# Kernel tuning notes

Hardware: AMD Instinct MI355X
Metric: run time of the kernel (lower is better)

The kernel has to match this reference:

```python
import jax, jax.numpy as jnp
import numpy as np

B, S, D, H, DF = 8, 1024, 1024, 16, 4096
DK = D // H
EPS = 1e-5


def setup_inputs() -> dict:
    key = jax.random.key(0)
    ks = jax.random.split(key, 16)
    w = lambda k, shape: (jax.random.normal(k, shape, jnp.float32) * 0.02)
    inp = {
        "x": jax.random.normal(ks[0], (B, S, D), jnp.float32),
        "mask": jnp.ones((B, 1, 1, S), jnp.int32),
        # attention projections (torch Linear: y = x @ W.T + b)
        "Wq": w(ks[1], (D, D)), "bq": jnp.zeros((D,), jnp.float32),
        "Wk": w(ks[2], (D, D)), "bk": jnp.zeros((D,), jnp.float32),
        "Wv": w(ks[3], (D, D)), "bv": jnp.zeros((D,), jnp.float32),
        "Wo": w(ks[4], (D, D)), "bo": jnp.zeros((D,), jnp.float32),
        "ln_attn_g": jnp.ones((D,), jnp.float32), "ln_attn_b": jnp.zeros((D,), jnp.float32),
        # feed-forward
        "W1": w(ks[5], (DF, D)), "b1": jnp.zeros((DF,), jnp.float32),
        "W2": w(ks[6], (D, DF)), "b2": jnp.zeros((D,), jnp.float32),
        "ln_ff_g": jnp.ones((D,), jnp.float32), "ln_ff_b": jnp.zeros((D,), jnp.float32),
        # BatchNorm1d(d_ff) inside FFN (eval mode: running stats)
        "bnff_g": jnp.ones((DF,), jnp.float32), "bnff_b": jnp.zeros((DF,), jnp.float32),
        "bnff_m": jnp.zeros((DF,), jnp.float32), "bnff_v": jnp.ones((DF,), jnp.float32),
        # BatchNorm1d(d_model) after each sublayer (eval mode)
        "bn1_g": jnp.ones((D,), jnp.float32), "bn1_b": jnp.zeros((D,), jnp.float32),
        "bn1_m": jnp.zeros((D,), jnp.float32), "bn1_v": jnp.ones((D,), jnp.float32),
        "bn2_g": jnp.ones((D,), jnp.float32), "bn2_b": jnp.zeros((D,), jnp.float32),
        "bn2_m": jnp.zeros((D,), jnp.float32), "bn2_v": jnp.ones((D,), jnp.float32),
    }
    return inp


def _layernorm(x, g, b):
    mu = jnp.mean(x, axis=-1, keepdims=True)
    var = jnp.mean(jnp.square(x - mu), axis=-1, keepdims=True)
    return (x - mu) * jax.lax.rsqrt(var + EPS) * g + b


def _batchnorm_eval(x, g, b, m, v):
    # x: [B,S,C]; BatchNorm1d over channel C (the transpose->bn->transpose in torch
    # is equivalent to per-channel affine normalization on the last dim in eval mode)
    return (x - m) * jax.lax.rsqrt(v + EPS) * g + b


def reference(x, mask, Wq, bq, Wk, bk, Wv, bv, Wo, bo, ln_attn_g, ln_attn_b,
              W1, b1, W2, b2, ln_ff_g, ln_ff_b,
              bnff_g, bnff_b, bnff_m, bnff_v,
              bn1_g, bn1_b, bn1_m, bn1_v,
              bn2_g, bn2_b, bn2_m, bn2_v):
    # ---- Multi-head self-attention (pre-LN on query/key/value input) ----
    xq = _layernorm(x, ln_attn_g, ln_attn_b)
    q = (xq @ Wq.T + bq).reshape(B, S, H, DK)
    k = (x @ Wk.T + bk).reshape(B, S, H, DK)   # note: original applies LN only to `query`;
    v = (x @ Wv.T + bv).reshape(B, S, H, DK)   # key/value are passed raw (same x here)
    scores = jnp.einsum("bqhd,bkhd->bhqk", q, k) / np.sqrt(DK).astype(np.float32)
    scores = jnp.where(mask == 0, jnp.float32(-1e9), scores)
    attn = jax.nn.softmax(scores, axis=-1)                      # [B,H,S,S]
    context = jnp.einsum("bhqk,bkhd->bqhd", attn, v).reshape(B, S, D)
    attn_out = context @ Wo.T + bo
    x = x + attn_out                                            # residual (eval: no dropout)
    x = _batchnorm_eval(x, bn1_g, bn1_b, bn1_m, bn1_v)
    # ---- Position-wise FFN ----
    xn = _layernorm(x, ln_ff_g, ln_ff_b)
    h = jax.nn.gelu(xn @ W1.T + b1, approximate=False)          # [B,S,DF]
    h = _batchnorm_eval(h, bnff_g, bnff_b, bnff_m, bnff_v)
    ff = h @ W2.T + b2
    x = x + ff
    x = _batchnorm_eval(x, bn2_g, bn2_b, bn2_m, bn2_v)
    return x, attn
```

## Files before the change

### kernel.cpp

```cpp
#include <hip/hip_runtime.h>
#include <hip/hip_bf16.h>
#include <math.h>

typedef __hip_bfloat16 bf16;
typedef __attribute__((ext_vector_type(8))) short short8;
typedef __attribute__((ext_vector_type(4))) short short4v;
typedef __attribute__((ext_vector_type(4))) float f32x4;

#define DEV static __device__ __forceinline__

DEV short f2bf(float f) {
    bf16 h = __float2bfloat16(f);
    return __builtin_bit_cast(short, h);
}

DEV void glds16(const void* g, void* l) {
    __builtin_amdgcn_global_load_lds((const __attribute__((address_space(1))) void*)g,
                                     (__attribute__((address_space(3))) void*)l, 16, 0, 0);
}

__global__ __launch_bounds__(256) void cast_all(const float* __restrict__ Wq,
                                                const float* __restrict__ Wk,
                                                const float* __restrict__ Wv,
                                                const float* __restrict__ Wo,
                                                const float* __restrict__ W1,
                                                const float* __restrict__ W2,
                                                bf16* __restrict__ wqkv, bf16* __restrict__ wo,
                                                bf16* __restrict__ w1, bf16* __restrict__ w2) {
    int i = blockIdx.x * 256 + threadIdx.x;
    const float* src;
    bf16* dst;
    int si, di;
    if (i < 786432) {
        src = (i < 262144) ? Wq : (i < 524288) ? Wk : Wv;
        si = (i < 262144) ? i : (i < 524288) ? i - 262144 : i - 524288;
        dst = wqkv; di = i;
    } else if (i < 1048576) {
        src = Wo; si = i - 786432; dst = wo; di = si;
    } else if (i < 2097152) {
        src = W1; si = i - 1048576; dst = w1; di = si;
    } else {
        src = W2; si = i - 2097152; dst = w2; di = si;
    }
    f32x4 v = ((const f32x4*)src)[si];
    short4v o;
    #pragma unroll
    for (int j = 0; j < 4; j++) o[j] = f2bf(v[j]);
    ((short4v*)dst)[di] = o;
}

__global__ __launch_bounds__(256) void affine_all(
    const float* __restrict__ g1, const float* __restrict__ bb1, const float* __restrict__ m1, const float* __restrict__ v1,
    const float* __restrict__ g2, const float* __restrict__ bb2, const float* __restrict__ m2, const float* __restrict__ v2,
    const float* __restrict__ gf, const float* __restrict__ bbf, const float* __restrict__ mf, const float* __restrict__ vf,
    float* __restrict__ s1, float* __restrict__ t1, float* __restrict__ s2, float* __restrict__ t2,
    float* __restrict__ sf, float* __restrict__ tf) {
    int i = blockIdx.x * 256 + threadIdx.x;
    const float *g, *b, *m, *v; float *s, *t; int j;
    if (i < 1024)      { g = g1; b = bb1; m = m1; v = v1; s = s1; t = t1; j = i; }
    else if (i < 2048) { g = g2; b = bb2; m = m2; v = v2; s = s2; t = t2; j = i - 1024; }
    else               { g = gf; b = bbf; m = mf; v = vf; s = sf; t = tf; j = i - 2048; }
    float sc = g[j] * rsqrtf(v[j] + 1e-5f);
    s[j] = sc;
    t[j] = b[j] - m[j] * sc;
}

__global__ __launch_bounds__(256) void ln_kernel(const float* __restrict__ x,
                                                 const float* __restrict__ g,
                                                 const float* __restrict__ b,
                                                 bf16* __restrict__ lnout,
                                                 bf16* __restrict__ rawout) {
    const int row = blockIdx.x, t = threadIdx.x;
    const float* xr = x + (size_t)row * 1024;
    f32x4 v = ((const f32x4*)xr)[t];
    float s = v[0] + v[1] + v[2] + v[3];
    float sq = v[0]*v[0] + v[1]*v[1] + v[2]*v[2] + v[3]*v[3];
    #pragma unroll
    for (int off = 1; off < 64; off <<= 1) {
        s  += __shfl_xor(s, off);
        sq += __shfl_xor(sq, off);
    }
    __shared__ float ls[4], lq[4];
    if ((t & 63) == 0) { ls[t >> 6] = s; lq[t >> 6] = sq; }
    __syncthreads();
    s = ls[0] + ls[1] + ls[2] + ls[3];
    sq = lq[0] + lq[1] + lq[2] + lq[3];
    float mu = s * (1.0f / 1024.0f);
    float rs = rsqrtf(sq * (1.0f / 1024.0f) - mu * mu + 1e-5f);
    f32x4 gg = ((const f32x4*)g)[t];
    f32x4 bb = ((const f32x4*)b)[t];
    short4v o;
    #pragma unroll
    for (int j = 0; j < 4; j++) o[j] = f2bf((v[j] - mu) * rs * gg[j] + bb[j]);
    ((short4v*)(lnout + (size_t)row * 1024))[t] = o;
    if (rawout) {
        short4v r;
        #pragma unroll
        for (int j = 0; j < 4; j++) r[j] = f2bf(v[j]);
        ((short4v*)(rawout + (size_t)row * 1024))[t] = r;
    }
}

enum { M_RESBN = 0, M_GELU = 1, M_QKV = 2 };

template <int BN, int MODE>
__global__ __launch_bounds__(512, 2) void gemm8(
    const bf16* __restrict__ A0, const bf16* __restrict__ A1, const bf16* __restrict__ Bw,
    const float* __restrict__ b0, const float* __restrict__ b1, const float* __restrict__ b2,
    void* __restrict__ o0, void* __restrict__ o1, void* __restrict__ o2,
    const float* __restrict__ res, const float* __restrict__ sa, const float* __restrict__ ta,
    int N, int K) {
    constexpr int NB = BN / 64;
    constexpr int SB = BN * 128;
    constexpr int CW = BN / 4;
    constexpr int NF = CW / 16;
    __shared__ char smem[65536 + 2 * SB];

    const int tid = threadIdx.x, lane = tid & 63, wid = tid >> 6;
    const int gx = gridDim.x;
    const int n_wg = gx * gridDim.y;
    int lin = blockIdx.y * gx + blockIdx.x;
    lin = (lin & 7) * (n_wg >> 3) + (lin >> 3);
    const int bn = (lin % gx) * BN, bm = (lin / gx) << 8;

    const int wr = wid >> 2, wc = wid & 3;
    const int arow = lane & 15, hi = lane >> 4;
    const int xr = arow & 7;
    const int ck0 = (hi ^ xr) << 3;
    const int ck1 = ((4 + hi) ^ xr) << 3;
    const int rowA = wr * 128 + arow;
    const int rowB = wc * CW + arow;

    const bf16* Asel;
    if constexpr (MODE == M_QKV) Asel = (bn < 1024) ? A0 : A1;
    else                         Asel = A0;

    const int rS = tid >> 3;
    const int cXor = ((tid & 7) ^ (rS & 7)) << 3;
    const bf16* gA = Asel + (size_t)(bm + rS) * K + cXor;
    const bf16* gB = Bw   + (size_t)(bn + rS) * K + cXor;

    f32x4 acc[8][NF] = {};

    auto stA = [&](int t, int i) {
        glds16(gA + (size_t)i * 64 * K + t * 64,
               smem + ((t & 1) << 15) + i * 8192 + (wid << 10));
    };
    auto stB = [&](int t, int i) {
        glds16(gB + (size_t)i * 64 * K + t * 64,
               smem + 65536 + (t & 1) * SB + i * 8192 + (wid << 10));
    };

    const int NT = K >> 6;
    #pragma unroll
    for (int i = 0; i < NB; i++) stB(0, i);
    stA(0, 0); stA(0, 2); stA(0, 1); stA(0, 3);

#define PHASE(Q)                                                                              \
    do {                                                                                      \
        const short8 a00 = *(const short8*)(Ap + (rowA + (2*(Q)) * 16) * 64 + ck0);           \
        const short8 a01 = *(const short8*)(Ap + (rowA + (2*(Q)) * 16) * 64 + ck1);           \
        const short8 a10 = *(const short8*)(Ap + (rowA + (2*(Q)+1) * 16) * 64 + ck0);         \
        const short8 a11 = *(const short8*)(Ap + (rowA + (2*(Q)+1) * 16) * 64 + ck1);         \
        __builtin_amdgcn_s_setprio(1);                                                        \
        _Pragma("unroll")                                                                     \
        for (int n = 0; n < NF; n++) {                                                        \
            acc[2*(Q)][n]   = __builtin_amdgcn_mfma_f32_16x16x32_bf16(a00, bva[n], acc[2*(Q)][n], 0, 0, 0);   \
            acc[2*(Q)][n]   = __builtin_amdgcn_mfma_f32_16x16x32_bf16(a01, bvb[n], acc[2*(Q)][n], 0, 0, 0);   \
            acc[2*(Q)+1][n] = __builtin_amdgcn_mfma_f32_16x16x32_bf16(a10, bva[n], acc[2*(Q)+1][n], 0, 0, 0); \
            acc[2*(Q)+1][n] = __builtin_amdgcn_mfma_f32_16x16x32_bf16(a11, bvb[n], acc[2*(Q)+1][n], 0, 0, 0); \
        }                                                                                     \
        __builtin_amdgcn_s_setprio(0);                                                        \
    } while (0)

    for (int t = 0; t < NT; ++t) {
        const int p = t & 1;
        const bf16* Ap = (const bf16*)(smem + (p << 15));
        const bf16* Bp = (const bf16*)(smem + 65536 + p * SB);
        asm volatile("s_waitcnt vmcnt(2)" ::: "memory");
        __builtin_amdgcn_s_barrier();
        if (t + 1 < NT) {
            stB(t + 1, 0);
            if constexpr (NB == 4) stB(t + 1, 1);
        }
        short8 bva[NF], bvb[NF];
        #pragma unroll
        for (int n = 0; n < NF; n++) {
            bva[n] = *(const short8*)(Bp + (rowB + n * 16) * 64 + ck0);
            bvb[n] = *(const short8*)(Bp + (rowB + n * 16) * 64 + ck1);
        }
        PHASE(0);
        __builtin_amdgcn_s_barrier();
        if (t + 1 < NT) {
            if constexpr (NB == 4) { stB(t + 1, 2); stB(t + 1, 3); }
            else                   { stB(t + 1, 1); }
        }
        PHASE(1);
        if (t == NT - 1) asm volatile("s_waitcnt vmcnt(0)" ::: "memory");
        else if constexpr (NB == 4) asm volatile("s_waitcnt vmcnt(4)" ::: "memory");
        else                        asm volatile("s_waitcnt vmcnt(2)" ::: "memory");
        __builtin_amdgcn_s_barrier();
        if (t + 1 < NT) { stA(t + 1, 0); stA(t + 1, 2); }
        PHASE(2);
        __builtin_amdgcn_s_barrier();
        if (t + 1 < NT) { stA(t + 1, 1); stA(t + 1, 3); }
        PHASE(3);
    }
#undef PHASE

    #pragma unroll
    for (int mf = 0; mf < 8; mf++) {
        #pragma unroll
        for (int nf = 0; nf < NF; nf++) {
            const int col = bn + wc * CW + nf * 16 + arow;
            #pragma unroll
            for (int j = 0; j < 4; j++) {
                const int row = bm + wr * 128 + mf * 16 + hi * 4 + j;
                if constexpr (MODE == M_RESBN) {
                    float v = acc[mf][nf][j] + b0[col];
                    size_t idx = (size_t)row * N + col;
                    ((float*)o0)[idx] = (res[idx] + v) * sa[col] + ta[col];
                } else if constexpr (MODE == M_GELU) {
                    float v = acc[mf][nf][j] + b0[col];
                    float ge = 0.5f * v * (1.0f + erff(v * 0.70710678118f));
                    ((bf16*)o0)[(size_t)row * N + col] = __float2bfloat16(ge * sa[col] + ta[col]);
                } else {
                    const int reg = col >> 10, c = col & 1023;
                    const float bb = (reg == 0) ? b0[c] : (reg == 1) ? b1[c] : b2[c];
                    float v = acc[mf][nf][j] + bb;
                    if (reg == 0)
                        ((bf16*)o0)[(size_t)row * 1024 + c] = __float2bfloat16(v * 0.125f);
                    else if (reg == 1)
                        ((bf16*)o1)[(size_t)row * 1024 + c] = __float2bfloat16(v);
                    else
                        ((bf16*)o2)[((size_t)(row >> 10) << 20) + ((size_t)c << 10) + (row & 1023)] =
                            __float2bfloat16(v);
                }
            }
        }
    }
}

__global__ __launch_bounds__(512, 4) void fattn_kernel(const bf16* __restrict__ q,
                                                       const bf16* __restrict__ k,
                                                       const bf16* __restrict__ vT,
                                                       const int* __restrict__ mask,
                                                       float* __restrict__ attn,
                                                       bf16* __restrict__ ctx) {
    const int bh = blockIdx.y, b = bh >> 4, h = bh & 15;
    const int q0 = blockIdx.x << 5;
    const int tid = threadIdx.x, lane = tid & 63, wid = tid >> 6;
    const int kb = wid << 7;
    const int arow = lane & 15, hi = lane >> 4, koff = hi << 3;
    const int rbase = hi << 2;

    __shared__ char smem[67584];
    bf16* Plds = (bf16*)smem;
    float* redm = (float*)(smem + 65536);
    float* reds = (float*)(smem + 66560);

    const size_t obase = (((size_t)bh << 10) + q0) << 10;

    for (int m = 0; m < 2; m++) {
        const bf16* qp = q + ((size_t)((b << 10) + q0 + (m << 4) + arow) << 10) + (h << 6);
        const short8 qf  = *(const short8*)(qp + koff);
        const short8 qf2 = *(const short8*)(qp + 32 + koff);

        f32x4 acc[8];
        #pragma unroll
        for (int n = 0; n < 8; n++) acc[n] = (f32x4){0.f, 0.f, 0.f, 0.f};

        #pragma unroll
        for (int n = 0; n < 8; n++) {
            const bf16* kp = k + ((size_t)((b << 10) + kb + (n << 4) + arow) << 10) + (h << 6);
            short8 kf  = *(const short8*)(kp + koff);
            short8 kf2 = *(const short8*)(kp + 32 + koff);
            acc[n] = __builtin_amdgcn_mfma_f32_16x16x32_bf16(qf,  kf,  acc[n], 0, 0, 0);
            acc[n] = __builtin_amdgcn_mfma_f32_16x16x32_bf16(qf2, kf2, acc[n], 0, 0, 0);
        }

        float rmax[4];
        #pragma unroll
        for (int j = 0; j < 4; j++) rmax[j] = -3.0e38f;
        #pragma unroll
        for (int n = 0; n < 8; n++) {
            const float madd = mask[(b << 10) + kb + (n << 4) + arow] ? 0.0f : -1e9f;
            #pragma unroll
            for (int j = 0; j < 4; j++) {
                acc[n][j] += madd;
                rmax[j] = fmaxf(rmax[j], acc[n][j]);
            }
        }
        #pragma unroll
        for (int off = 1; off < 16; off <<= 1)
            #pragma unroll
            for (int j = 0; j < 4; j++) rmax[j] = fmaxf(rmax[j], __shfl_xor(rmax[j], off));

        if (arow == 0) {
            #pragma unroll
            for (int j = 0; j < 4; j++) redm[(((m << 4) + rbase + j) << 3) + wid] = rmax[j];
        }
        __syncthreads();
        #pragma unroll
        for (int j = 0; j < 4; j++) {
            const float* rr = redm + (((m << 4) + rbase + j) << 3);
            f32x4 r0 = *(const f32x4*)rr, r1 = *(const f32x4*)(rr + 4);
            rmax[j] = fmaxf(fmaxf(fmaxf(r0[0], r0[1]), fmaxf(r0[2], r0[3])),
                            fmaxf(fmaxf(r1[0], r1[1]), fmaxf(r1[2], r1[3])));
        }

        float rsum[4] = {0.f, 0.f, 0.f, 0.f};
        #pragma unroll
        for (int n = 0; n < 8; n++)
            #pragma unroll
            for (int j = 0; j < 4; j++) {
                float p = __expf(acc[n][j] - rmax[j]);
                acc[n][j] = p;
                rsum[j] += p;
            }
        #pragma unroll
        for (int off = 1; off < 16; off <<= 1)
            #pragma unroll
            for (int j = 0; j < 4; j++) rsum[j] += __shfl_xor(rsum[j], off);

        if (arow == 0) {
            #pragma unroll
            for (int j = 0; j < 4; j++) reds[(((m << 4) + rbase + j) << 3) + wid] = rsum[j];
        }
        __syncthreads();
        float inv[4];
        #pragma unroll
        for (int j = 0; j < 4; j++) {
            const float* rr = reds + (((m << 4) + rbase + j) << 3);
            f32x4 r0 = *(const f32x4*)rr, r1 = *(const f32x4*)(rr + 4);
            inv[j] = 1.0f / (r0[0] + r0[1] + r0[2] + r0[3] + r1[0] + r1[1] + r1[2] + r1[3]);
        }

        #pragma unroll
        for (int j = 0; j < 4; j++) {
            const int qr = (m << 4) + rbase + j;
            float* orow = attn + obase + ((size_t)qr << 10) + kb;
            char* prow = (char*)Plds + (qr << 11);
            const int rx = (qr & 7) << 4;
            const float iv = inv[j];
            #pragma unroll
            for (int n = 0; n < 8; n++) {
                float p = acc[n][j] * iv;
                orow[(n << 4) + arow] = p;
                *(bf16*)(prow + ((((kb + (n << 4) + arow)) << 1) ^ rx)) = __float2bfloat16(p);
            }
        }
    }

    asm volatile("s_waitcnt lgkmcnt(0)" ::: "memory");
    __builtin_amdgcn_s_barrier();
    __builtin_amdgcn_sched_barrier(0);

    const int qh = wid >> 2, dh = wid & 3;
    const char* pbase = (char*)Plds + (((qh << 4) + arow) << 11);
    const int prx = (arow & 7) << 4;
    const bf16* vrow = vT + ((size_t)((b << 10) + (h << 6) + (dh << 4) + arow) << 10);
    f32x4 acc2 = (f32x4){0.f, 0.f, 0.f, 0.f};
    #pragma unroll 8
    for (int kt = 0; kt < 32; kt++) {
        short8 af  = *(const short8*)(pbase + (((kt << 6) + (hi << 4)) ^ prx));
        short8 bf2 = *(const short8*)(vrow + (kt << 5) + koff);
        acc2 = __builtin_amdgcn_mfma_f32_16x16x32_bf16(af, bf2, acc2, 0, 0, 0);
    }

    #pragma unroll
    for (int j = 0; j < 4; j++) {
        const int row = q0 + (qh << 4) + rbase + j;
        ctx[((size_t)((b << 10) + row) << 10) + (h << 6) + (dh << 4) + arow] =
            __float2bfloat16(acc2[j]);
    }
}

extern "C" void kernel_launch(void* const* d_in, const int* in_sizes, int n_in,
                              void* d_out, int out_size, void* d_ws, size_t ws_size,
                              hipStream_t stream) {
    (void)in_sizes; (void)n_in; (void)out_size; (void)ws_size;
    const float* x   = (const float*)d_in[0];
    const int*   mask= (const int*)d_in[1];
    const float* Wq  = (const float*)d_in[2];  const float* bq  = (const float*)d_in[3];
    const float* Wk  = (const float*)d_in[4];  const float* bk  = (const float*)d_in[5];
    const float* Wv  = (const float*)d_in[6];  const float* bv  = (const float*)d_in[7];
    const float* Wo  = (const float*)d_in[8];  const float* bo  = (const float*)d_in[9];
    const float* lag = (const float*)d_in[10]; const float* lab = (const float*)d_in[11];
    const float* W1  = (const float*)d_in[12]; const float* b1  = (const float*)d_in[13];
    const float* W2  = (const float*)d_in[14]; const float* b2  = (const float*)d_in[15];
    const float* lfg = (const float*)d_in[16]; const float* lfb = (const float*)d_in[17];
    const float* bffg= (const float*)d_in[18]; const float* bffb= (const float*)d_in[19];
    const float* bffm= (const float*)d_in[20]; const float* bffv= (const float*)d_in[21];
    const float* b1g = (const float*)d_in[22]; const float* b1b = (const float*)d_in[23];
    const float* b1m = (const float*)d_in[24]; const float* b1v = (const float*)d_in[25];
    const float* b2g = (const float*)d_in[26]; const float* b2b = (const float*)d_in[27];
    const float* b2m = (const float*)d_in[28]; const float* b2v = (const float*)d_in[29];

    char* ws = (char*)d_ws;
    const size_t MB = 1024 * 1024;
    bf16* wqkv_bf = (bf16*)(ws);
    bf16* wo_bf   = (bf16*)(ws + 6 * MB);
    bf16* w1_bf   = (bf16*)(ws + 8 * MB);
    bf16* w2_bf   = (bf16*)(ws + 16 * MB);
    float* s1  = (float*)(ws + 24 * MB); float* t1  = s1 + 1024;
    float* s2  = t1 + 1024;              float* t2  = s2 + 1024;
    float* sff = t2 + 1024;              float* tff = sff + 4096;
    bf16* x_bf   = (bf16*)(ws + 25 * MB);
    bf16* xq_bf  = (bf16*)(ws + 41 * MB);
    bf16* q_bf   = (bf16*)(ws + 57 * MB);
    bf16* k_bf   = (bf16*)(ws + 73 * MB);
    bf16* vT_bf  = (bf16*)(ws + 89 * MB);
    bf16* ctx_bf = (bf16*)(ws + 105 * MB);
    float* x1    = (float*)(ws + 121 * MB);
    bf16* xn_bf  = (bf16*)(ws + 153 * MB);
    bf16* h_bf   = (bf16*)(ws + 169 * MB);

    float* out_x    = (float*)d_out;
    float* out_attn = out_x + (size_t)8 * 1024 * 1024;

    cast_all<<<12288, 256, 0, stream>>>(Wq, Wk, Wv, Wo, W1, W2, wqkv_bf, wo_bf, w1_bf, w2_bf);
    affine_all<<<24, 256, 0, stream>>>(b1g, b1b, b1m, b1v, b2g, b2b, b2m, b2v,
                                       bffg, bffb, bffm, bffv, s1, t1, s2, t2, sff, tff);

    ln_kernel<<<8192, 256, 0, stream>>>(x, lag, lab, xq_bf, x_bf);

    gemm8<128, M_QKV><<<dim3(24, 32), 512, 0, stream>>>(
        xq_bf, x_bf, wqkv_bf, bq, bk, bv, q_bf, k_bf, vT_bf, nullptr, nullptr, nullptr, 1024, 1024);

    fattn_kernel<<<dim3(32, 128), 512, 0, stream>>>(q_bf, k_bf, vT_bf, mask, out_attn, ctx_bf);

    gemm8<128, M_RESBN><<<dim3(8, 32), 512, 0, stream>>>(
        ctx_bf, nullptr, wo_bf, bo, nullptr, nullptr, x1, nullptr, nullptr, x, s1, t1, 1024, 1024);

    ln_kernel<<<8192, 256, 0, stream>>>(x1, lfg, lfb, xn_bf, nullptr);
    gemm8<256, M_GELU><<<dim3(16, 32), 512, 0, stream>>>(
        xn_bf, nullptr, w1_bf, b1, nullptr, nullptr, h_bf, nullptr, nullptr, nullptr, sff, tff, 4096, 1024);
    gemm8<128, M_RESBN><<<dim3(8, 32), 512, 0, stream>>>(
        h_bf, nullptr, w2_bf, b2, nullptr, nullptr, out_x, nullptr, nullptr, x1, s2, t2, 1024, 4096);
}
```

Baseline: 729.1 us.

## Restructure attention blocks to 16 query rows with single-barrier online softmax merge

The attention kernel now uses 256-thread blocks handling 16 query rows, with each of 4 waves covering 256 keys, instead of 512 threads over 32 rows in two passes. The max and sum reductions across waves are merged into one barrier using a log-sum-exp rescale, which removes one of the two cross-wave syncs per row tile. K fragment loads are software-prefetched one step ahead of the MFMAs. Each wave holds 16 accumulator tiles, which raises register pressure, and the grid doubles in size.

```diff
diff --git a/kernel.cpp b/kernel.cpp
--- a/kernel.cpp
+++ b/kernel.cpp
@@ -241,114 +241,114 @@
     }
 }
 
-__global__ __launch_bounds__(512, 4) void fattn_kernel(const bf16* __restrict__ q,
+__global__ __launch_bounds__(256, 4) void fattn_kernel(const bf16* __restrict__ q,
                                                        const bf16* __restrict__ k,
                                                        const bf16* __restrict__ vT,
                                                        const int* __restrict__ mask,
                                                        float* __restrict__ attn,
                                                        bf16* __restrict__ ctx) {
     const int bh = blockIdx.y, b = bh >> 4, h = bh & 15;
-    const int q0 = blockIdx.x << 5;
+    const int q0 = blockIdx.x << 4;
     const int tid = threadIdx.x, lane = tid & 63, wid = tid >> 6;
-    const int kb = wid << 7;
+    const int kb = wid << 8;
     const int arow = lane & 15, hi = lane >> 4, koff = hi << 3;
     const int rbase = hi << 2;
 
-    __shared__ char smem[67584];
+    __shared__ char smem[33280];
     bf16* Plds = (bf16*)smem;
-    float* redm = (float*)(smem + 65536);
-    float* reds = (float*)(smem + 66560);
+    float* redm = (float*)(smem + 32768);
+    float* reds = (float*)(smem + 33024);
+
+    const bf16* qp = q + ((size_t)((b << 10) + q0 + arow) << 10) + (h << 6);
+    const short8 qf  = *(const short8*)(qp + koff);
+    const short8 qf2 = *(const short8*)(qp + 32 + koff);
+
+    f32x4 acc[16];
+    #pragma unroll
+    for (int n = 0; n < 16; n++) acc[n] = (f32x4){0.f, 0.f, 0.f, 0.f};
+
+    const bf16* kpBase = k + ((size_t)((b << 10) + kb + arow) << 10) + (h << 6);
+    short8 kf  = *(const short8*)(kpBase + koff);
+    short8 kf2 = *(const short8*)(kpBase + 32 + koff);
+    #pragma unroll
+    for (int n = 0; n < 16; n++) {
+        short8 kfn, kf2n;
+        if (n < 15) {
+            const bf16* kp = kpBase + ((size_t)(n + 1) << 14);
+            kfn  = *(const short8*)(kp + koff);
+            kf2n = *(const short8*)(kp + 32 + koff);
+        }
+        acc[n] = __builtin_amdgcn_mfma_f32_16x16x32_bf16(qf,  kf,  acc[n], 0, 0, 0);
+        acc[n] = __builtin_amdgcn_mfma_f32_16x16x32_bf16(qf2, kf2, acc[n], 0, 0, 0);
+        kf = kfn; kf2 = kf2n;
+    }
+
+    float rmax[4];
+    #pragma unroll
+    for (int j = 0; j < 4; j++) rmax[j] = -3.0e38f;
+    #pragma unroll
+    for (int n = 0; n < 16; n++) {
+        const float madd = mask[(b << 10) + kb + (n << 4) + arow] ? 0.0f : -1e9f;
+        #pragma unroll
+        for (int j = 0; j < 4; j++) {
+            acc[n][j] += madd;
+            rmax[j] = fmaxf(rmax[j], acc[n][j]);
+        }
+    }
+    #pragma unroll
+    for (int off = 1; off < 16; off <<= 1)
+        #pragma unroll
+        for (int j = 0; j < 4; j++) rmax[j] = fmaxf(rmax[j], __shfl_xor(rmax[j], off));
+
+    float rsum[4] = {0.f, 0.f, 0.f, 0.f};
+    #pragma unroll
+    for (int n = 0; n < 16; n++)
+        #pragma unroll
+        for (int j = 0; j < 4; j++) {
+            float p = __expf(acc[n][j] - rmax[j]);
+            acc[n][j] = p;
+            rsum[j] += p;
+        }
+    #pragma unroll
+    for (int off = 1; off < 16; off <<= 1)
+        #pragma unroll
+        for (int j = 0; j < 4; j++) rsum[j] += __shfl_xor(rsum[j], off);
+
+    if (arow == 0) {
+        #pragma unroll
+        for (int j = 0; j < 4; j++) {
+            const int qr = rbase + j;
+            redm[(qr << 2) + wid] = rmax[j];
+            reds[(qr << 2) + wid] = rsum[j];
+        }
+    }
+    __syncthreads();
+
+    float fscale[4];
+    #pragma unroll
+    for (int j = 0; j < 4; j++) {
+        const int qr = rbase + j;
+        f32x4 m0 = *(const f32x4*)(redm + (qr << 2));
+        f32x4 s0 = *(const f32x4*)(reds + (qr << 2));
+        float gm = fmaxf(fmaxf(m0[0], m0[1]), fmaxf(m0[2], m0[3]));
+        float S = s0[0] * __expf(m0[0] - gm) + s0[1] * __expf(m0[1] - gm) +
+                  s0[2] * __expf(m0[2] - gm) + s0[3] * __expf(m0[3] - gm);
+        fscale[j] = __expf(rmax[j] - gm) / S;
+    }
 
     const size_t obase = (((size_t)bh << 10) + q0) << 10;
-
-    for (int m = 0; m < 2; m++) {
-        const bf16* qp = q + ((size_t)((b << 10) + q0 + (m << 4) + arow) << 10) + (h << 6);
-        const short8 qf  = *(const short8*)(qp + koff);
-        const short8 qf2 = *(const short8*)(qp + 32 + koff);
-
-        f32x4 acc[8];
-        #pragma unroll
-        for (int n = 0; n < 8; n++) acc[n] = (f32x4){0.f, 0.f, 0.f, 0.f};
-
-        #pragma unroll
-        for (int n = 0; n < 8; n++) {
-            const bf16* kp = k + ((size_t)((b << 10) + kb + (n << 4) + arow) << 10) + (h << 6);
-            short8 kf  = *(const short8*)(kp + koff);
-            short8 kf2 = *(const short8*)(kp + 32 + koff);
-            acc[n] = __builtin_amdgcn_mfma_f32_16x16x32_bf16(qf,  kf,  acc[n], 0, 0, 0);
-            acc[n] = __builtin_amdgcn_mfma_f32_16x16x32_bf16(qf2, kf2, acc[n], 0, 0, 0);
-        }
-
-        float rmax[4];
-        #pragma unroll
-        for (int j = 0; j < 4; j++) rmax[j] = -3.0e38f;
-        #pragma unroll
-        for (int n = 0; n < 8; n++) {
-            const float madd = mask[(b << 10) + kb + (n << 4) + arow] ? 0.0f : -1e9f;
-            #pragma unroll
-            for (int j = 0; j < 4; j++) {
-                acc[n][j] += madd;
-                rmax[j] = fmaxf(rmax[j], acc[n][j]);
-            }
-        }
-        #pragma unroll
-        for (int off = 1; off < 16; off <<= 1)
-            #pragma unroll
-            for (int j = 0; j < 4; j++) rmax[j] = fmaxf(rmax[j], __shfl_xor(rmax[j], off));
-
-        if (arow == 0) {
-            #pragma unroll
-            for (int j = 0; j < 4; j++) redm[(((m << 4) + rbase + j) << 3) + wid] = rmax[j];
-        }
-        __syncthreads();
-        #pragma unroll
-        for (int j = 0; j < 4; j++) {
-            const float* rr = redm + (((m << 4) + rbase + j) << 3);
-            f32x4 r0 = *(const f32x4*)rr, r1 = *(const f32x4*)(rr + 4);
-            rmax[j] = fmaxf(fmaxf(fmaxf(r0[0], r0[1]), fmaxf(r0[2], r0[3])),
-                            fmaxf(fmaxf(r1[0], r1[1]), fmaxf(r1[2], r1[3])));
-        }
-
-        float rsum[4] = {0.f, 0.f, 0.f, 0.f};
-        #pragma unroll
-        for (int n = 0; n < 8; n++)
-            #pragma unroll
-            for (int j = 0; j < 4; j++) {
-                float p = __expf(acc[n][j] - rmax[j]);
-                acc[n][j] = p;
-                rsum[j] += p;
-            }
-        #pragma unroll
-        for (int off = 1; off < 16; off <<= 1)
-            #pragma unroll
-            for (int j = 0; j < 4; j++) rsum[j] += __shfl_xor(rsum[j], off);
-
-        if (arow == 0) {
-            #pragma unroll
-            for (int j = 0; j < 4; j++) reds[(((m << 4) + rbase + j) << 3) + wid] = rsum[j];
-        }
-        __syncthreads();
-        float inv[4];
-        #pragma unroll
-        for (int j = 0; j < 4; j++) {
-            const float* rr = reds + (((m << 4) + rbase + j) << 3);
-            f32x4 r0 = *(const f32x4*)rr, r1 = *(const f32x4*)(rr + 4);
-            inv[j] = 1.0f / (r0[0] + r0[1] + r0[2] + r0[3] + r1[0] + r1[1] + r1[2] + r1[3]);
-        }
-
-        #pragma unroll
-        for (int j = 0; j < 4; j++) {
-            const int qr = (m << 4) + rbase + j;
-            float* orow = attn + obase + ((size_t)qr << 10) + kb;
-            char* prow = (char*)Plds + (qr << 11);
-            const int rx = (qr & 7) << 4;
-            const float iv = inv[j];
-            #pragma unroll
-            for (int n = 0; n < 8; n++) {
-                float p = acc[n][j] * iv;
-                orow[(n << 4) + arow] = p;
-                *(bf16*)(prow + ((((kb + (n << 4) + arow)) << 1) ^ rx)) = __float2bfloat16(p);
-            }
+    #pragma unroll
+    for (int j = 0; j < 4; j++) {
+        const int qr = rbase + j;
+        float* orow = attn + obase + ((size_t)qr << 10) + kb;
+        char* prow = (char*)Plds + (qr << 11);
+        const int rx = (qr & 7) << 4;
+        const float iv = fscale[j];
+        #pragma unroll
+        for (int n = 0; n < 16; n++) {
+            float p = acc[n][j] * iv;
+            orow[(n << 4) + arow] = p;
+            *(bf16*)(prow + ((((kb + (n << 4) + arow)) << 1) ^ rx)) = __float2bfloat16(p);
         }
     }
 
@@ -356,8 +356,8 @@
     __builtin_amdgcn_s_barrier();
     __builtin_amdgcn_sched_barrier(0);
 
-    const int qh = wid >> 2, dh = wid & 3;
-    const char* pbase = (char*)Plds + (((qh << 4) + arow) << 11);
+    const int dh = wid;
+    const char* pbase = (char*)Plds + (arow << 11);
     const int prx = (arow & 7) << 4;
     const bf16* vrow = vT + ((size_t)((b << 10) + (h << 6) + (dh << 4) + arow) << 10);
     f32x4 acc2 = (f32x4){0.f, 0.f, 0.f, 0.f};
@@ -370,7 +370,7 @@
 
     #pragma unroll
     for (int j = 0; j < 4; j++) {
-        const int row = q0 + (qh << 4) + rbase + j;
+        const int row = q0 + rbase + j;
         ctx[((size_t)((b << 10) + row) << 10) + (h << 6) + (dh << 4) + arow] =
             __float2bfloat16(acc2[j]);
     }
@@ -428,7 +428,7 @@
     gemm8<128, M_QKV><<<dim3(24, 32), 512, 0, stream>>>(
         xq_bf, x_bf, wqkv_bf, bq, bk, bv, q_bf, k_bf, vT_bf, nullptr, nullptr, nullptr, 1024, 1024);
 
-    fattn_kernel<<<dim3(32, 128), 512, 0, stream>>>(q_bf, k_bf, vT_bf, mask, out_attn, ctx_bf);
+    fattn_kernel<<<dim3(64, 128), 256, 0, stream>>>(q_bf, k_bf, vT_bf, mask, out_attn, ctx_bf);
 
     gemm8<128, M_RESBN><<<dim3(8, 32), 512, 0, stream>>>(
         ctx_bf, nullptr, wo_bf, bo, nullptr, nullptr, x1, nullptr, nullptr, x, s1, t1, 1024, 1024);
```

New measurement: 656.6 us. 9.9% less time.
